# Kernel optimization log

Hardware: AMD Instinct MI355X
Metric: run time of the kernel (lower is better)

## Reference

```python
import jax, jax.numpy as jnp
import numpy as np
import math

D_MODEL = 512
NUM_HEADS = 8
D_HEAD = D_MODEL // NUM_HEADS
B, S = 4, 2048
L = 2 * S - 1  # relative position range


def _rel_shift(pos_score):
    # pos_score: [B, H, S, L] -> [B, H, S, L//2+1] via pad/reshape/slice trick
    b, h, s, l = pos_score.shape
    padded = jnp.pad(pos_score, ((0, 0), (0, 0), (0, 0), (1, 0)))  # [B,H,S,L+1]
    padded = padded.reshape(b, h, l + 1, s)
    shifted = padded[:, :, 1:].reshape(b, h, s, l)
    return shifted[..., : l // 2 + 1]


def setup_inputs() -> dict:
    key = jax.random.key(0)
    ks = jax.random.split(key, 16)
    std = 1.0 / math.sqrt(D_MODEL)
    inp = {
        "query": jax.random.normal(ks[0], (B, S, D_MODEL), jnp.float32),
        "key": jax.random.normal(ks[1], (B, S, D_MODEL), jnp.float32),
        "value": jax.random.normal(ks[2], (B, S, D_MODEL), jnp.float32),
        "pos_embedding": jax.random.normal(ks[3], (B, L, D_MODEL), jnp.float32),
        "Wq": jax.random.normal(ks[4], (D_MODEL, D_MODEL), jnp.float32) * std,
        "bq": jnp.zeros((D_MODEL,), jnp.float32),
        "Wk": jax.random.normal(ks[5], (D_MODEL, D_MODEL), jnp.float32) * std,
        "bk": jnp.zeros((D_MODEL,), jnp.float32),
        "Wv": jax.random.normal(ks[6], (D_MODEL, D_MODEL), jnp.float32) * std,
        "bv": jnp.zeros((D_MODEL,), jnp.float32),
        "Wp": jax.random.normal(ks[7], (D_MODEL, D_MODEL), jnp.float32) * std,
        "u_bias": jax.random.normal(ks[8], (NUM_HEADS, D_HEAD), jnp.float32) * std,
        "v_bias": jax.random.normal(ks[9], (NUM_HEADS, D_HEAD), jnp.float32) * std,
        "Wo": jax.random.normal(ks[10], (D_MODEL, D_MODEL), jnp.float32) * std,
        "bo": jnp.zeros((D_MODEL,), jnp.float32),
    }
    return inp


def reference(query, key, value, pos_embedding, Wq, bq, Wk, bk, Wv, bv, Wp, u_bias, v_bias, Wo, bo):
    b, s, d = query.shape
    h, dh = u_bias.shape
    sqrt_dim = jnp.asarray(math.sqrt(d), query.dtype)

    q = (query @ Wq.T + bq).reshape(b, s, h, dh)
    k = (key @ Wk.T + bk).reshape(b, -1, h, dh)
    v = (value @ Wv.T + bv).reshape(b, -1, h, dh)
    p = (pos_embedding @ Wp.T).reshape(b, -1, h, dh)

    content_score = jnp.einsum("bshd,bthd->bhst", q + u_bias, k)
    pos_score = jnp.einsum("bshd,blhd->bhsl", q + v_bias, p)
    pos_score = _rel_shift(pos_score)  # [B,H,S,S]

    score = (content_score + pos_score) / sqrt_dim
    attn = jax.nn.softmax(score, axis=-1)
    context = jnp.einsum("bhst,bthd->bshd", attn, v).reshape(b, s, d)
    return context @ Wo.T + bo
```

## Files before the change

### kernel.cpp

```cpp
#include <hip/hip_runtime.h>


typedef __bf16 bf16;
typedef __bf16 bf16x4 __attribute__((ext_vector_type(4)));
typedef __bf16 bf16x8 __attribute__((ext_vector_type(8)));
typedef float  f32x4  __attribute__((ext_vector_type(4)));

#define MFMA(A,B,C) __builtin_amdgcn_mfma_f32_16x16x32_bf16((A),(B),(C),0,0,0)

constexpr float SCP = 1.44269504088896f / 22.6274169979695f;

__device__ __forceinline__ void gload16(const void* g, void* l) {
    __builtin_amdgcn_global_load_lds(
        (const __attribute__((address_space(1))) void*)g,
        (__attribute__((address_space(3))) void*)l, 16, 0, 0);
}

constexpr size_t WBYTES   = 512u*512u*2u;
constexpr size_t OFF_WQ   = 0;
constexpr size_t OFF_WK   = OFF_WQ + WBYTES;
constexpr size_t OFF_WV   = OFF_WK + WBYTES;
constexpr size_t OFF_WP   = OFF_WV + WBYTES;
constexpr size_t OFF_WO   = OFF_WP + WBYTES;
constexpr size_t QKV_BYTES = 4ull*8*2048*64*2;
constexpr size_t OFF_QU   = OFF_WO + WBYTES;
constexpr size_t OFF_QV   = OFF_QU + QKV_BYTES;
constexpr size_t OFF_KK   = OFF_QV + QKV_BYTES;
constexpr size_t OFF_VT   = OFF_KK + QKV_BYTES;
constexpr size_t OFF_PP   = OFF_VT + QKV_BYTES;
constexpr size_t PP_BYTES = 4ull*8*4096*64*2;
constexpr size_t OFF_CTX  = OFF_PP + PP_BYTES;

__global__ __launch_bounds__(256) void convert_weights(
    const float* __restrict__ w0, const float* __restrict__ w1,
    const float* __restrict__ w2, const float* __restrict__ w3,
    const float* __restrict__ w4, bf16* __restrict__ dst)
{
    int idx = blockIdx.x * 256 + threadIdx.x;
    const float* srcs[5] = {w0, w1, w2, w3, w4};
    int which = idx >> 15;
    int off   = (idx & 32767) * 8;
    const float* s = srcs[which] + off;
    float4 a = *(const float4*)s;
    float4 b = *(const float4*)(s + 4);
    bf16x8 o;
    o[0]=(bf16)a.x; o[1]=(bf16)a.y; o[2]=(bf16)a.z; o[3]=(bf16)a.w;
    o[4]=(bf16)b.x; o[5]=(bf16)b.y; o[6]=(bf16)b.z; o[7]=(bf16)b.w;
    *(bf16x8*)(dst + (size_t)which * (512*512) + off) = o;
}

__global__ __launch_bounds__(256) void gemm_proj(
    const float* __restrict__ Aq, const float* __restrict__ Ak,
    const float* __restrict__ Av, const float* __restrict__ Ap,
    const bf16* __restrict__ Wqb, const bf16* __restrict__ Wkb,
    const bf16* __restrict__ Wvb, const bf16* __restrict__ Wpb,
    const float* __restrict__ bq, const float* __restrict__ bk,
    const float* __restrict__ bv,
    const float* __restrict__ ub, const float* __restrict__ vb,
    bf16* __restrict__ qu, bf16* __restrict__ qv, bf16* __restrict__ kk,
    bf16* __restrict__ vt, bf16* __restrict__ pp)
{
    const int bid = blockIdx.x;
    const int mode = (bid < 768) ? (bid >> 8) : 3;
    const int idx  = (bid < 768) ? (bid & 255) : (bid - 768);
    const float* A  = (mode == 0) ? Aq  : (mode == 1) ? Ak  : (mode == 2) ? Av  : Ap;
    const bf16*  Bw = (mode == 0) ? Wqb : (mode == 1) ? Wkb : (mode == 2) ? Wvb : Wpb;

    __shared__ __align__(16) bf16 As[128 * 64];
    const int tid = threadIdx.x, lane = tid & 63, w = tid >> 6;
    const int r = lane & 15, g = lane >> 4;
    const int m0 = (idx >> 2) * 128, n0 = (idx & 3) * 128;
    const int wr = (w >> 1) * 64, wc = (w & 1) * 64;
    f32x4 acc[4][4] = {};

    for (int kt = 0; kt < 512; kt += 64) {
        __syncthreads();
        #pragma unroll
        for (int i = 0; i < 4; i++) {
            int gi = tid + 256 * i;
            int row = gi >> 3, c8 = gi & 7;
            int gm = m0 + row;
            float4 a0 = {0,0,0,0}, a1 = {0,0,0,0};
            if (mode != 3 || gm < 16380) {
                const float* ap = A + (size_t)gm * 512 + kt + c8 * 8;
                a0 = *(const float4*)ap;
                a1 = *(const float4*)(ap + 4);
            }
            bf16x8 v8;
            v8[0]=(bf16)a0.x; v8[1]=(bf16)a0.y; v8[2]=(bf16)a0.z; v8[3]=(bf16)a0.w;
            v8[4]=(bf16)a1.x; v8[5]=(bf16)a1.y; v8[6]=(bf16)a1.z; v8[7]=(bf16)a1.w;
            *(bf16x8*)((char*)As + row * 128 + ((c8 ^ (row & 7)) << 4)) = v8;
        }
        __syncthreads();
        #pragma unroll
        for (int ks = 0; ks < 2; ks++) {
            bf16x8 af[4], bfr[4];
            #pragma unroll
            for (int rt = 0; rt < 4; rt++) {
                int row = wr + rt * 16 + r;
                af[rt] = *(const bf16x8*)((const char*)As + row * 128 +
                                          (((ks * 4 + g) ^ (row & 7)) << 4));
            }
            #pragma unroll
            for (int ct = 0; ct < 4; ct++) {
                int n = n0 + wc + ct * 16 + r;
                bfr[ct] = *(const bf16x8*)(Bw + (size_t)n * 512 + kt + ks * 32 + g * 8);
            }
            #pragma unroll
            for (int rt = 0; rt < 4; rt++)
                #pragma unroll
                for (int ct = 0; ct < 4; ct++)
                    acc[rt][ct] = MFMA(af[rt], bfr[ct], acc[rt][ct]);
        }
    }

    #pragma unroll
    for (int rt = 0; rt < 4; rt++) {
        #pragma unroll
        for (int ct = 0; ct < 4; ct++) {
            int gn = n0 + wc + ct * 16 + r;
            int rb = m0 + wr + rt * 16 + g * 4;
            #pragma unroll
            for (int i = 0; i < 4; i++) {
                int gm = rb + i;
                float val = acc[rt][ct][i];
                if (mode == 0) {
                    int b = gm >> 11, s = gm & 2047, h = gn >> 6, dh = gn & 63;
                    size_t o = ((size_t)((b * 8 + h) * 2048 + s)) * 64 + dh;
                    float qb = val + bq[gn];
                    qu[o] = (bf16)((qb + ub[gn]) * SCP);
                    qv[o] = (bf16)((qb + vb[gn]) * SCP);
                } else if (mode == 1) {
                    int b = gm >> 11, s = gm & 2047, h = gn >> 6, dh = gn & 63;
                    kk[((size_t)((b * 8 + h) * 2048 + s)) * 64 +
                       (dh ^ ((s & 7) << 3))] = (bf16)(val + bk[gn]);
                } else if (mode == 2) {
                    int b = gm >> 11, s = gm & 2047, h = gn >> 6, dh = gn & 63;
                    int sc = s & 63, sb = s & ~63;
                    vt[((size_t)((b * 8 + h) * 64 + dh)) * 2048 + sb +
                       (sc ^ ((dh & 7) << 3))] = (bf16)(val + bv[gn]);
                } else {
                    if (gm < 16380) {
                        int b = gm / 4095, l = gm - b * 4095, h = gn >> 6, dh = gn & 63;
                        pp[((size_t)((b * 8 + h) * 4096 + l)) * 64 + dh] = (bf16)val;
                    }
                }
            }
        }
    }
}

__global__ __launch_bounds__(256) void gemm_out(
    const bf16* __restrict__ Ac, const bf16* __restrict__ Bw,
    const float* __restrict__ bias, float* __restrict__ of)
{
    __shared__ __align__(16) bf16 As[128 * 64];
    const int tid = threadIdx.x, lane = tid & 63, w = tid >> 6;
    const int r = lane & 15, g = lane >> 4;
    const int m0 = blockIdx.x * 128, n0 = blockIdx.y * 128;
    const int wr = (w >> 1) * 64, wc = (w & 1) * 64;
    f32x4 acc[4][4] = {};

    for (int kt = 0; kt < 512; kt += 64) {
        __syncthreads();
        #pragma unroll
        for (int i = 0; i < 4; i++) {
            int gi = tid + 256 * i;
            int row = gi >> 3, c8 = gi & 7;
            bf16x8 v8 = *(const bf16x8*)(Ac + (size_t)(m0 + row) * 512 + kt + c8 * 8);
            *(bf16x8*)((char*)As + row * 128 + ((c8 ^ (row & 7)) << 4)) = v8;
        }
        __syncthreads();
        #pragma unroll
        for (int ks = 0; ks < 2; ks++) {
            bf16x8 af[4], bfr[4];
            #pragma unroll
            for (int rt = 0; rt < 4; rt++) {
                int row = wr + rt * 16 + r;
                af[rt] = *(const bf16x8*)((const char*)As + row * 128 +
                                          (((ks * 4 + g) ^ (row & 7)) << 4));
            }
            #pragma unroll
            for (int ct = 0; ct < 4; ct++) {
                int n = n0 + wc + ct * 16 + r;
                bfr[ct] = *(const bf16x8*)(Bw + (size_t)n * 512 + kt + ks * 32 + g * 8);
            }
            #pragma unroll
            for (int rt = 0; rt < 4; rt++)
                #pragma unroll
                for (int ct = 0; ct < 4; ct++)
                    acc[rt][ct] = MFMA(af[rt], bfr[ct], acc[rt][ct]);
        }
    }
    #pragma unroll
    for (int rt = 0; rt < 4; rt++)
        #pragma unroll
        for (int ct = 0; ct < 4; ct++) {
            int gn = n0 + wc + ct * 16 + r;
            int rb = m0 + wr + rt * 16 + g * 4;
            #pragma unroll
            for (int i = 0; i < 4; i++)
                of[(size_t)(rb + i) * 512 + gn] = acc[rt][ct][i] + bias[gn];
        }
}

__global__ __launch_bounds__(512, 4) void attn_k(
    const bf16* __restrict__ qu, const bf16* __restrict__ qv,
    const bf16* __restrict__ kk, const bf16* __restrict__ vt,
    const bf16* __restrict__ pp, bf16* __restrict__ ctx)
{
    __shared__ __align__(16) bf16 kls[2][64 * 64];
    __shared__ __align__(16) bf16 vls[3][64 * 64];
    __shared__ __align__(16) bf16 ps2[128][84];
    __shared__ __align__(16) bf16 at_t[128 * 64];

    const int lane = threadIdx.x & 63, w = threadIdx.x >> 6;
    const int r = lane & 15, g = lane >> 4;
    const int sw = (r & 7) << 4;
    const int bid = blockIdx.x;
    const int lbid = (bid & 7) * 64 + (bid >> 3);
    const int bh = lbid >> 4;
    const int sigma = lbid & 15;
    const int s0 = sigma << 7;

    const bf16* quB = qu + (size_t)bh * 2048 * 64;
    const bf16* qvB = qv + (size_t)bh * 2048 * 64;
    const bf16* kkB = kk + (size_t)bh * 2048 * 64;
    const bf16* vtB = vt + (size_t)bh * 64 * 2048;
    const bf16* ppB = pp + (size_t)bh * 4096 * 64;

    bf16x8 qaf0, qaf1, qvf0, qvf1;
    {
        const int srow = s0 + 16 * w + r;
        qaf0 = *(const bf16x8*)(quB + (size_t)srow * 64 + g * 8);
        qaf1 = *(const bf16x8*)(quB + (size_t)srow * 64 + 32 + g * 8);
        qvf0 = *(const bf16x8*)(qvB + (size_t)srow * 64 + g * 8);
        qvf1 = *(const bf16x8*)(qvB + (size_t)srow * 64 + 32 + g * 8);
    }
    __builtin_amdgcn_sched_barrier(0);

    bf16* psR = &ps2[16 * w + r][0];
    const int lq = lane >> 3, lc = (lane & 7) << 4;

    bf16x8 pfP[10];
    {
        const int tp = ((sigma * 2) & 31) << 6;
        gload16((const char*)kkB + ((size_t)(tp + w * 8 + lq) << 7) + lc,
                (char*)kls[0] + w * 1024);
        gload16((const char*)vtB + ((size_t)(w * 8 + lq) << 12) + tp * 2 + lc,
                (char*)vls[0] + w * 1024);
        __builtin_amdgcn_sched_barrier(0);
        const int lbw = tp - s0 + 2032 - 16 * w;
        #pragma unroll
        for (int j = 0; j < 5; j++) {
            const bf16* pr = ppB + (size_t)(lbw + j * 16 + r) * 64 + g * 8;
            pfP[2*j]   = *(const bf16x8*)pr;
            pfP[2*j+1] = *(const bf16x8*)(pr + 32);
        }
        asm volatile("s_waitcnt vmcnt(0)" ::: "memory");
        __builtin_amdgcn_s_barrier();
        __builtin_amdgcn_sched_barrier(0);
    }

    f32x4 oacc[4] = {};
    float sum = 0.f;
    int iv_prev = 2, iv_cur = 0, iv_next = 1;

    #pragma unroll 2
    for (int n = 0; n < 32; ++n) {
        const int cur = n & 1;
        if (n > 0) {
            __builtin_amdgcn_s_barrier();
            __builtin_amdgcn_sched_barrier(0);
        }

        {
            const int tn = ((sigma * 2 + n + 1) & 31) << 6;
            gload16((const char*)kkB + ((size_t)(tn + w * 8 + lq) << 7) + lc,
                    (char*)kls[cur ^ 1] + w * 1024);
            gload16((const char*)vtB + ((size_t)(w * 8 + lq) << 12) + tn * 2 + lc,
                    (char*)vls[iv_next] + w * 1024);
        }
        __builtin_amdgcn_sched_barrier(0);

        if (n > 0) {
            const char* vbase = (const char*)vls[iv_prev];
            bf16x8 af0 = *(const bf16x8*)((const char*)at_t + (16 * w + r) * 128 +
                                          ((0 + g * 16) ^ sw));
            bf16x8 af1 = *(const bf16x8*)((const char*)at_t + (16 * w + r) * 128 +
                                          ((64 + g * 16) ^ sw));
            #pragma unroll
            for (int nt = 0; nt < 4; nt++) {
                const char* vb_ = vbase + (nt * 16 + r) * 128;
                bf16x8 vf0 = *(const bf16x8*)(vb_ + (( 0 + g * 16) ^ sw));
                bf16x8 vf1 = *(const bf16x8*)(vb_ + ((64 + g * 16) ^ sw));
                oacc[nt] = MFMA(af0, vf0, oacc[nt]);
                oacc[nt] = MFMA(af1, vf1, oacc[nt]);
            }
        }

        #pragma unroll
        for (int j = 0; j < 5; j++) {
            f32x4 ps = {};
            ps = MFMA(pfP[2*j],   qvf0, ps);
            ps = MFMA(pfP[2*j+1], qvf1, ps);
            bf16x4 pb;
            pb[0]=(bf16)ps[0]; pb[1]=(bf16)ps[1]; pb[2]=(bf16)ps[2]; pb[3]=(bf16)ps[3];
            *(bf16x4*)(psR + j * 16 + g * 4) = pb;
        }

        {
            const int tn  = ((sigma * 2 + n + 1) & 31) << 6;
            const int lbw = tn - s0 + 2032 - 16 * w;
            #pragma unroll
            for (int j = 0; j < 5; j++) {
                const bf16* pr = ppB + (size_t)(lbw + j * 16 + r) * 64 + g * 8;
                pfP[2*j]   = *(const bf16x8*)pr;
                pfP[2*j+1] = *(const bf16x8*)(pr + 32);
            }
        }

        f32x4 cc[4];
        #pragma unroll
        for (int c = 0; c < 4; c++) {
            const char* kb = (const char*)kls[cur] + (c * 16 + r) * 128;
            bf16x8 k0 = *(const bf16x8*)(kb + (( 0 + g * 16) ^ sw));
            bf16x8 k1 = *(const bf16x8*)(kb + ((64 + g * 16) ^ sw));
            f32x4 a = {};
            a = MFMA(k0, qaf0, a);
            a = MFMA(k1, qaf1, a);
            cc[c] = a;
        }

        #pragma unroll
        for (int c = 0; c < 4; c++) {
            const int base = c * 16 + g * 4 + 15 - r;
            float p0 = psR[base], p1 = psR[base+1], p2 = psR[base+2], p3 = psR[base+3];
            float e0 = exp2f(cc[c][0] + p0);
            float e1 = exp2f(cc[c][1] + p1);
            float e2 = exp2f(cc[c][2] + p2);
            float e3 = exp2f(cc[c][3] + p3);
            sum += (e0 + e1) + (e2 + e3);
            bf16x4 pk;
            pk[0]=(bf16)e0; pk[1]=(bf16)e1; pk[2]=(bf16)e2; pk[3]=(bf16)e3;
            *(bf16x4*)((char*)at_t + (16 * w + r) * 128 + ((c * 32 + g * 8) ^ sw)) = pk;
        }

        #pragma unroll
        for (int j = 0; j < 10; j++)
            asm volatile("" : "+v"(pfP[j]));

        const int t_ = iv_prev; iv_prev = iv_cur; iv_cur = iv_next; iv_next = t_;
    }

    asm volatile("s_waitcnt vmcnt(0)" ::: "memory");

    {
        const char* vbase = (const char*)vls[iv_prev];
        bf16x8 af0 = *(const bf16x8*)((const char*)at_t + (16 * w + r) * 128 +
                                      ((0 + g * 16) ^ sw));
        bf16x8 af1 = *(const bf16x8*)((const char*)at_t + (16 * w + r) * 128 +
                                      ((64 + g * 16) ^ sw));
        #pragma unroll
        for (int nt = 0; nt < 4; nt++) {
            const char* vb_ = vbase + (nt * 16 + r) * 128;
            bf16x8 vf0 = *(const bf16x8*)(vb_ + (( 0 + g * 16) ^ sw));
            bf16x8 vf1 = *(const bf16x8*)(vb_ + ((64 + g * 16) ^ sw));
            oacc[nt] = MFMA(af0, vf0, oacc[nt]);
            oacc[nt] = MFMA(af1, vf1, oacc[nt]);
        }
    }

    sum += __shfl_xor(sum, 16);
    sum += __shfl_xor(sum, 32);
    const float inv = 1.f / sum;

    const int b = bh >> 3, h = bh & 7;
    #pragma unroll
    for (int nt = 0; nt < 4; nt++) {
        #pragma unroll
        for (int i = 0; i < 4; i++) {
            const float si = __shfl(inv, g * 4 + i);
            const int s = s0 + 16 * w + g * 4 + i;
            const int col = h * 64 + nt * 16 + r;
            ctx[((size_t)(b * 2048 + s)) * 512 + col] = (bf16)(oacc[nt][i] * si);
        }
    }
}

extern "C" void kernel_launch(void* const* d_in, const int* in_sizes, int n_in,
                              void* d_out, int out_size, void* d_ws, size_t ws_size,
                              hipStream_t stream)
{
    (void)in_sizes; (void)n_in; (void)out_size; (void)ws_size;
    const float* query = (const float*)d_in[0];
    const float* key_  = (const float*)d_in[1];
    const float* value = (const float*)d_in[2];
    const float* pos   = (const float*)d_in[3];
    const float* Wq = (const float*)d_in[4];  const float* bq = (const float*)d_in[5];
    const float* Wk = (const float*)d_in[6];  const float* bk = (const float*)d_in[7];
    const float* Wv = (const float*)d_in[8];  const float* bv = (const float*)d_in[9];
    const float* Wp = (const float*)d_in[10];
    const float* ub = (const float*)d_in[11]; const float* vb = (const float*)d_in[12];
    const float* Wo = (const float*)d_in[13]; const float* bo = (const float*)d_in[14];

    char* ws = (char*)d_ws;
    bf16* Wqb = (bf16*)(ws + OFF_WQ);
    bf16* Wkb = (bf16*)(ws + OFF_WK);
    bf16* Wvb = (bf16*)(ws + OFF_WV);
    bf16* Wpb = (bf16*)(ws + OFF_WP);
    bf16* Wob = (bf16*)(ws + OFF_WO);
    bf16* quP = (bf16*)(ws + OFF_QU);
    bf16* qvP = (bf16*)(ws + OFF_QV);
    bf16* kkP = (bf16*)(ws + OFF_KK);
    bf16* vtP = (bf16*)(ws + OFF_VT);
    bf16* ppP = (bf16*)(ws + OFF_PP);
    bf16* ctxP = (bf16*)(ws + OFF_CTX);

    convert_weights<<<640, 256, 0, stream>>>(Wq, Wk, Wv, Wp, Wo, (bf16*)(ws + OFF_WQ));

    gemm_proj<<<dim3(1280), 256, 0, stream>>>(
        query, key_, value, pos, Wqb, Wkb, Wvb, Wpb,
        bq, bk, bv, ub, vb, quP, qvP, kkP, vtP, ppP);

    attn_k<<<dim3(512), 512, 0, stream>>>(quP, qvP, kkP, vtP, ppP, ctxP);

    gemm_out<<<dim3(64, 4), 256, 0, stream>>>(ctxP, Wob, bo, (float*)d_out);
}
```

Before: 292.5 us.

## Double query rows per attention block to reuse K/V tiles across two subtiles

Each attention workgroup now handles 256 query rows instead of 128, with each wave owning two 16-row query subtiles. Every K, V and position-embedding fragment loaded into LDS or registers now feeds twice as many MFMAs, which halves global K/V traffic per query. The grid shrinks to 256 blocks, the launch bound drops to 2 waves per SIMD, and register and LDS use grow, so occupancy and latency hiding may suffer and only 256 blocks are available to fill the GPU.

```diff
diff --git a/kernel.cpp b/kernel.cpp
--- a/kernel.cpp
+++ b/kernel.cpp
@@ -204,24 +204,25 @@
         }
 }
 
-__global__ __launch_bounds__(512, 4) void attn_k(
+__global__ __launch_bounds__(512, 2) void attn_k(
     const bf16* __restrict__ qu, const bf16* __restrict__ qv,
     const bf16* __restrict__ kk, const bf16* __restrict__ vt,
     const bf16* __restrict__ pp, bf16* __restrict__ ctx)
 {
     __shared__ __align__(16) bf16 kls[2][64 * 64];
     __shared__ __align__(16) bf16 vls[3][64 * 64];
-    __shared__ __align__(16) bf16 ps2[128][84];
-    __shared__ __align__(16) bf16 at_t[128 * 64];
+    __shared__ __align__(16) bf16 ps2[256][100];
+    __shared__ __align__(16) bf16 at_t[256 * 64];
 
     const int lane = threadIdx.x & 63, w = threadIdx.x >> 6;
     const int r = lane & 15, g = lane >> 4;
     const int sw = (r & 7) << 4;
     const int bid = blockIdx.x;
-    const int lbid = (bid & 7) * 64 + (bid >> 3);
-    const int bh = lbid >> 4;
-    const int sigma = lbid & 15;
-    const int s0 = sigma << 7;
+    const int lbid = (bid & 7) * 32 + (bid >> 3);
+    const int bh = lbid >> 3;
+    const int sigma = lbid & 7;
+    const int s0 = sigma << 8;
+    const int qb = w << 5;
 
     const bf16* quB = qu + (size_t)bh * 2048 * 64;
     const bf16* qvB = qv + (size_t)bh * 2048 * 64;
@@ -229,30 +230,30 @@
     const bf16* vtB = vt + (size_t)bh * 64 * 2048;
     const bf16* ppB = pp + (size_t)bh * 4096 * 64;
 
-    bf16x8 qaf0, qaf1, qvf0, qvf1;
+    bf16x8 qaf[2][2], qvf[2][2];
+    #pragma unroll
+    for (int qs = 0; qs < 2; qs++) {
+        const int srow = s0 + qb + qs * 16 + r;
+        qaf[qs][0] = *(const bf16x8*)(quB + (size_t)srow * 64 + g * 8);
+        qaf[qs][1] = *(const bf16x8*)(quB + (size_t)srow * 64 + 32 + g * 8);
+        qvf[qs][0] = *(const bf16x8*)(qvB + (size_t)srow * 64 + g * 8);
+        qvf[qs][1] = *(const bf16x8*)(qvB + (size_t)srow * 64 + 32 + g * 8);
+    }
+    __builtin_amdgcn_sched_barrier(0);
+
+    const int lq = lane >> 3, lc = (lane & 7) << 4;
+
+    bf16x8 pfP[12];
     {
-        const int srow = s0 + 16 * w + r;
-        qaf0 = *(const bf16x8*)(quB + (size_t)srow * 64 + g * 8);
-        qaf1 = *(const bf16x8*)(quB + (size_t)srow * 64 + 32 + g * 8);
-        qvf0 = *(const bf16x8*)(qvB + (size_t)srow * 64 + g * 8);
-        qvf1 = *(const bf16x8*)(qvB + (size_t)srow * 64 + 32 + g * 8);
-    }
-    __builtin_amdgcn_sched_barrier(0);
-
-    bf16* psR = &ps2[16 * w + r][0];
-    const int lq = lane >> 3, lc = (lane & 7) << 4;
-
-    bf16x8 pfP[10];
-    {
-        const int tp = ((sigma * 2) & 31) << 6;
+        const int tp = ((sigma * 4) & 31) << 6;
         gload16((const char*)kkB + ((size_t)(tp + w * 8 + lq) << 7) + lc,
                 (char*)kls[0] + w * 1024);
         gload16((const char*)vtB + ((size_t)(w * 8 + lq) << 12) + tp * 2 + lc,
                 (char*)vls[0] + w * 1024);
         __builtin_amdgcn_sched_barrier(0);
-        const int lbw = tp - s0 + 2032 - 16 * w;
-        #pragma unroll
-        for (int j = 0; j < 5; j++) {
+        const int lbw = tp - s0 - qb + 2016;
+        #pragma unroll
+        for (int j = 0; j < 6; j++) {
             const bf16* pr = ppB + (size_t)(lbw + j * 16 + r) * 64 + g * 8;
             pfP[2*j]   = *(const bf16x8*)pr;
             pfP[2*j+1] = *(const bf16x8*)(pr + 32);
@@ -262,8 +263,8 @@
         __builtin_amdgcn_sched_barrier(0);
     }
 
-    f32x4 oacc[4] = {};
-    float sum = 0.f;
+    f32x4 oacc[2][4] = {};
+    float sums[2] = {0.f, 0.f};
     int iv_prev = 2, iv_cur = 0, iv_next = 1;
 
     #pragma unroll 2
@@ -275,7 +276,7 @@
         }
 
         {
-            const int tn = ((sigma * 2 + n + 1) & 31) << 6;
+            const int tn = ((sigma * 4 + n + 1) & 31) << 6;
             gload16((const char*)kkB + ((size_t)(tn + w * 8 + lq) << 7) + lc,
                     (char*)kls[cur ^ 1] + w * 1024);
             gload16((const char*)vtB + ((size_t)(w * 8 + lq) << 12) + tn * 2 + lc,
@@ -285,69 +286,83 @@
 
         if (n > 0) {
             const char* vbase = (const char*)vls[iv_prev];
-            bf16x8 af0 = *(const bf16x8*)((const char*)at_t + (16 * w + r) * 128 +
-                                          ((0 + g * 16) ^ sw));
-            bf16x8 af1 = *(const bf16x8*)((const char*)at_t + (16 * w + r) * 128 +
-                                          ((64 + g * 16) ^ sw));
-            #pragma unroll
-            for (int nt = 0; nt < 4; nt++) {
-                const char* vb_ = vbase + (nt * 16 + r) * 128;
-                bf16x8 vf0 = *(const bf16x8*)(vb_ + (( 0 + g * 16) ^ sw));
-                bf16x8 vf1 = *(const bf16x8*)(vb_ + ((64 + g * 16) ^ sw));
-                oacc[nt] = MFMA(af0, vf0, oacc[nt]);
-                oacc[nt] = MFMA(af1, vf1, oacc[nt]);
-            }
-        }
-
-        #pragma unroll
-        for (int j = 0; j < 5; j++) {
-            f32x4 ps = {};
-            ps = MFMA(pfP[2*j],   qvf0, ps);
-            ps = MFMA(pfP[2*j+1], qvf1, ps);
-            bf16x4 pb;
-            pb[0]=(bf16)ps[0]; pb[1]=(bf16)ps[1]; pb[2]=(bf16)ps[2]; pb[3]=(bf16)ps[3];
-            *(bf16x4*)(psR + j * 16 + g * 4) = pb;
+            #pragma unroll
+            for (int ks = 0; ks < 2; ks++) {
+                bf16x8 af[2];
+                #pragma unroll
+                for (int qs = 0; qs < 2; qs++)
+                    af[qs] = *(const bf16x8*)((const char*)at_t +
+                               (qb + qs * 16 + r) * 128 + ((ks * 64 + g * 16) ^ sw));
+                #pragma unroll
+                for (int nt = 0; nt < 4; nt++) {
+                    bf16x8 vf = *(const bf16x8*)(vbase + (nt * 16 + r) * 128 +
+                                                 ((ks * 64 + g * 16) ^ sw));
+                    oacc[0][nt] = MFMA(af[0], vf, oacc[0][nt]);
+                    oacc[1][nt] = MFMA(af[1], vf, oacc[1][nt]);
+                }
+            }
+        }
+
+        #pragma unroll
+        for (int j = 0; j < 6; j++) {
+            #pragma unroll
+            for (int qs = 0; qs < 2; qs++) {
+                f32x4 ps = {};
+                ps = MFMA(pfP[2*j],   qvf[qs][0], ps);
+                ps = MFMA(pfP[2*j+1], qvf[qs][1], ps);
+                bf16x4 pb;
+                pb[0]=(bf16)ps[0]; pb[1]=(bf16)ps[1]; pb[2]=(bf16)ps[2]; pb[3]=(bf16)ps[3];
+                *(bf16x4*)(&ps2[qb + qs * 16 + r][j * 16 + g * 4]) = pb;
+            }
         }
 
         {
-            const int tn  = ((sigma * 2 + n + 1) & 31) << 6;
-            const int lbw = tn - s0 + 2032 - 16 * w;
-            #pragma unroll
-            for (int j = 0; j < 5; j++) {
+            const int tn  = ((sigma * 4 + n + 1) & 31) << 6;
+            const int lbw = tn - s0 - qb + 2016;
+            #pragma unroll
+            for (int j = 0; j < 6; j++) {
                 const bf16* pr = ppB + (size_t)(lbw + j * 16 + r) * 64 + g * 8;
                 pfP[2*j]   = *(const bf16x8*)pr;
                 pfP[2*j+1] = *(const bf16x8*)(pr + 32);
             }
         }
 
-        f32x4 cc[4];
+        f32x4 cc[2][4];
         #pragma unroll
         for (int c = 0; c < 4; c++) {
             const char* kb = (const char*)kls[cur] + (c * 16 + r) * 128;
             bf16x8 k0 = *(const bf16x8*)(kb + (( 0 + g * 16) ^ sw));
             bf16x8 k1 = *(const bf16x8*)(kb + ((64 + g * 16) ^ sw));
-            f32x4 a = {};
-            a = MFMA(k0, qaf0, a);
-            a = MFMA(k1, qaf1, a);
-            cc[c] = a;
-        }
-
-        #pragma unroll
-        for (int c = 0; c < 4; c++) {
-            const int base = c * 16 + g * 4 + 15 - r;
-            float p0 = psR[base], p1 = psR[base+1], p2 = psR[base+2], p3 = psR[base+3];
-            float e0 = exp2f(cc[c][0] + p0);
-            float e1 = exp2f(cc[c][1] + p1);
-            float e2 = exp2f(cc[c][2] + p2);
-            float e3 = exp2f(cc[c][3] + p3);
-            sum += (e0 + e1) + (e2 + e3);
-            bf16x4 pk;
-            pk[0]=(bf16)e0; pk[1]=(bf16)e1; pk[2]=(bf16)e2; pk[3]=(bf16)e3;
-            *(bf16x4*)((char*)at_t + (16 * w + r) * 128 + ((c * 32 + g * 8) ^ sw)) = pk;
-        }
-
-        #pragma unroll
-        for (int j = 0; j < 10; j++)
+            #pragma unroll
+            for (int qs = 0; qs < 2; qs++) {
+                f32x4 a = {};
+                a = MFMA(k0, qaf[qs][0], a);
+                a = MFMA(k1, qaf[qs][1], a);
+                cc[qs][c] = a;
+            }
+        }
+
+        #pragma unroll
+        for (int qs = 0; qs < 2; qs++) {
+            const bf16* prow = &ps2[qb + qs * 16 + r][0];
+            #pragma unroll
+            for (int c = 0; c < 4; c++) {
+                const int base = c * 16 + g * 4 + 31 - qs * 16 - r;
+                float p0 = prow[base], p1 = prow[base+1], p2 = prow[base+2], p3 = prow[base+3];
+                float e0 = exp2f(cc[qs][c][0] + p0);
+                float e1 = exp2f(cc[qs][c][1] + p1);
+                float e2 = exp2f(cc[qs][c][2] + p2);
+                float e3 = exp2f(cc[qs][c][3] + p3);
+                sums[qs] += (e0 + e1) + (e2 + e3);
+                bf16x4 pk;
+                pk[0]=(bf16)e0; pk[1]=(bf16)e1; pk[2]=(bf16)e2; pk[3]=(bf16)e3;
+                *(bf16x4*)((char*)at_t + (qb + qs * 16 + r) * 128 +
+                           ((c * 32 + g * 8) ^ sw)) = pk;
+            }
+        }
+
+        #pragma unroll
+        for (int j = 0; j < 12; j++)
             asm volatile("" : "+v"(pfP[j]));
 
         const int t_ = iv_prev; iv_prev = iv_cur; iv_cur = iv_next; iv_next = t_;
@@ -357,33 +372,39 @@
 
     {
         const char* vbase = (const char*)vls[iv_prev];
-        bf16x8 af0 = *(const bf16x8*)((const char*)at_t + (16 * w + r) * 128 +
-                                      ((0 + g * 16) ^ sw));
-        bf16x8 af1 = *(const bf16x8*)((const char*)at_t + (16 * w + r) * 128 +
-                                      ((64 + g * 16) ^ sw));
-        #pragma unroll
-        for (int nt = 0; nt < 4; nt++) {
-            const char* vb_ = vbase + (nt * 16 + r) * 128;
-            bf16x8 vf0 = *(const bf16x8*)(vb_ + (( 0 + g * 16) ^ sw));
-            bf16x8 vf1 = *(const bf16x8*)(vb_ + ((64 + g * 16) ^ sw));
-            oacc[nt] = MFMA(af0, vf0, oacc[nt]);
-            oacc[nt] = MFMA(af1, vf1, oacc[nt]);
-        }
-    }
-
-    sum += __shfl_xor(sum, 16);
-    sum += __shfl_xor(sum, 32);
-    const float inv = 1.f / sum;
+        #pragma unroll
+        for (int ks = 0; ks < 2; ks++) {
+            bf16x8 af[2];
+            #pragma unroll
+            for (int qs = 0; qs < 2; qs++)
+                af[qs] = *(const bf16x8*)((const char*)at_t +
+                           (qb + qs * 16 + r) * 128 + ((ks * 64 + g * 16) ^ sw));
+            #pragma unroll
+            for (int nt = 0; nt < 4; nt++) {
+                bf16x8 vf = *(const bf16x8*)(vbase + (nt * 16 + r) * 128 +
+                                             ((ks * 64 + g * 16) ^ sw));
+                oacc[0][nt] = MFMA(af[0], vf, oacc[0][nt]);
+                oacc[1][nt] = MFMA(af[1], vf, oacc[1][nt]);
+            }
+        }
+    }
 
     const int b = bh >> 3, h = bh & 7;
     #pragma unroll
-    for (int nt = 0; nt < 4; nt++) {
-        #pragma unroll
-        for (int i = 0; i < 4; i++) {
-            const float si = __shfl(inv, g * 4 + i);
-            const int s = s0 + 16 * w + g * 4 + i;
-            const int col = h * 64 + nt * 16 + r;
-            ctx[((size_t)(b * 2048 + s)) * 512 + col] = (bf16)(oacc[nt][i] * si);
+    for (int qs = 0; qs < 2; qs++) {
+        float sm = sums[qs];
+        sm += __shfl_xor(sm, 16);
+        sm += __shfl_xor(sm, 32);
+        const float inv = 1.f / sm;
+        #pragma unroll
+        for (int nt = 0; nt < 4; nt++) {
+            #pragma unroll
+            for (int i = 0; i < 4; i++) {
+                const float si = __shfl(inv, g * 4 + i);
+                const int s = s0 + qb + qs * 16 + g * 4 + i;
+                const int col = h * 64 + nt * 16 + r;
+                ctx[((size_t)(b * 2048 + s)) * 512 + col] = (bf16)(oacc[qs][nt][i] * si);
+            }
         }
     }
 }
@@ -423,7 +444,7 @@
         query, key_, value, pos, Wqb, Wkb, Wvb, Wpb,
         bq, bk, bv, ub, vb, quP, qvP, kkP, vtP, ppP);
 
-    attn_k<<<dim3(512), 512, 0, stream>>>(quP, qvP, kkP, vtP, ppP, ctxP);
+    attn_k<<<dim3(256), 512, 0, stream>>>(quP, qvP, kkP, vtP, ppP, ctxP);
 
     gemm_out<<<dim3(64, 4), 256, 0, stream>>>(ctxP, Wob, bo, (float*)d_out);
 }
```

Result: faster. 255.1 us (-12.8%).
